# Optimization experiments

Hardware: AMD Instinct MI355X
Metric: run time of the kernel (lower is better)

The kernel has to match this reference:

```python
import jax, jax.numpy as jnp
import numpy as np

N_ATOMS, N_NBH, N_IN, N_FILTERS, N_OUT, N_GAUSS = 10000, 48, 128, 128, 128, 25
R_CUTOFF = 5.0
LOG2 = float(np.log(2.0))


def ssp(v):
    # shifted softplus, the SchNet activation
    return jax.nn.softplus(v) - LOG2


def setup_inputs() -> dict:
    key = jax.random.key(0)
    ks = jax.random.split(key, 10)
    x = jax.random.normal(ks[0], (N_ATOMS, N_IN), dtype=jnp.float32)
    dR = jax.random.uniform(ks[1], (N_ATOMS, N_NBH), dtype=jnp.float32) * 10.0  # distances in [0,10)
    dR_expanded = jax.random.normal(ks[2], (N_ATOMS, N_NBH, N_GAUSS), dtype=jnp.float32)
    pairwise_mask = jnp.ones((N_ATOMS, N_NBH), dtype=jnp.float32)
    neighbors_idx = jax.random.randint(ks[3], (N_ATOMS, N_NBH), 0, N_ATOMS, dtype=jnp.int32)
    s = 1.0 / np.sqrt(N_FILTERS)
    W1 = jax.random.normal(ks[4], (N_GAUSS, N_FILTERS), dtype=jnp.float32) * (1.0 / np.sqrt(N_GAUSS))
    b1 = jnp.zeros((N_FILTERS,), dtype=jnp.float32)
    W2 = jax.random.normal(ks[5], (N_FILTERS, N_FILTERS), dtype=jnp.float32) * s
    b2 = jnp.zeros((N_FILTERS,), dtype=jnp.float32)
    W_in2f = jax.random.normal(ks[6], (N_IN, N_FILTERS), dtype=jnp.float32) * (1.0 / np.sqrt(N_IN))
    W_f2out = jax.random.normal(ks[7], (N_FILTERS, N_OUT), dtype=jnp.float32) * s
    b_f2out = jnp.zeros((N_OUT,), dtype=jnp.float32)
    return {"x": x, "dR": dR, "dR_expanded": dR_expanded, "pairwise_mask": pairwise_mask,
            "neighbors_idx": neighbors_idx, "W1": W1, "b1": b1, "W2": W2, "b2": b2,
            "W_in2f": W_in2f, "W_f2out": W_f2out, "b_f2out": b_f2out}


def reference(x, dR, dR_expanded, pairwise_mask, neighbors_idx,
              W1, b1, W2, b2, W_in2f, W_f2out, b_f2out):
    # FilterNetwork: Dense + ssp + Dense, on Gaussian-smeared distances -> [N, K, F]
    W = jnp.einsum('nkg,gf->nkf', dR_expanded, W1) + b1
    W = jnp.einsum('nkf,fh->nkh', ssp(W), W2) + b2
    # HardCutoff: 1 where within cutoff
    C = (dR <= R_CUTOFF).astype(W.dtype)           # [N, K]
    W = W * C[..., None]
    # in2f (no bias), gather neighbor features
    y = x @ W_in2f                                  # [N, F]
    y = jnp.take(y, neighbors_idx, axis=0)          # [N, K, F] (gather == take_along_axis path)
    # filter-weighted multiply + masked sum aggregation over neighbor axis
    y = y * W
    y = jnp.sum(y * pairwise_mask[..., None], axis=1)  # [N, F]
    # f2out: Linear + shifted softplus
    return ssp(y @ W_f2out + b_f2out)               # [N, n_out]
```

## Files before the change

kernel.cpp:

```cpp
#include <hip/hip_runtime.h>
#include <hip/hip_bf16.h>


#define NA 10000
#define NK 48
#define NF 128
#define DREP 40
#define HP   136

typedef __bf16 bf16x8 __attribute__((ext_vector_type(8)));
typedef float  f32x4  __attribute__((ext_vector_type(4)));

__device__ __forceinline__ unsigned short f2bs(float x) {
    return __builtin_bit_cast(unsigned short, (__bf16)x);
}
__device__ __forceinline__ float bs2f(unsigned short u) {
    return (float)__builtin_bit_cast(__bf16, u);
}
__device__ __forceinline__ float sspf(float v) {
    return fmaxf(v, 0.0f) + __logf(1.0f + __expf(-fabsf(v))) - 0.69314718056f;
}

__global__ __launch_bounds__(256) void prep_weights(
    const float* __restrict__ W1,
    const float* __restrict__ W2,
    const float* __restrict__ Wi,
    unsigned short* __restrict__ wsb)
{
    int i = blockIdx.x * 256 + threadIdx.x;
    if (i < 4096) {
        int f = i >> 5, g = i & 31;
        wsb[i] = (g < 25) ? f2bs(W1[g * NF + f]) : (unsigned short)0;
    } else if (i < 20480) {
        int j = i - 4096; int h = j >> 7, k = j & 127;
        wsb[i] = f2bs(W2[k * NF + h]);
    } else if (i < 36864) {
        int j = i - 20480; int f = j >> 7, k = j & 127;
        wsb[i] = f2bs(Wi[k * NF + f]);
    }
}

__global__ __launch_bounds__(256) void in2f_mfma(
    const float* __restrict__ x,
    const unsigned short* __restrict__ WiT,
    unsigned short* __restrict__ yfeatb)
{
    const int tid = threadIdx.x;
    const int w = tid >> 6;
    const int lane = tid & 63;
    const int r = lane & 15;
    const int q = lane >> 4;
    const int m0 = blockIdx.x * 64 + w * 16;
    const int row = m0 + r;
    const bool rv = (row < NA);

    f32x4 acc[8];
    #pragma unroll
    for (int nt = 0; nt < 8; ++nt) { acc[nt][0]=0.f; acc[nt][1]=0.f; acc[nt][2]=0.f; acc[nt][3]=0.f; }

    #pragma unroll
    for (int ks = 0; ks < 4; ++ks) {
        bf16x8 a;
        if (rv) {
            const float4* xp = (const float4*)(x + (size_t)row * NF + ks * 32 + q * 8);
            float4 v0 = xp[0], v1 = xp[1];
            a[0]=(__bf16)v0.x; a[1]=(__bf16)v0.y; a[2]=(__bf16)v0.z; a[3]=(__bf16)v0.w;
            a[4]=(__bf16)v1.x; a[5]=(__bf16)v1.y; a[6]=(__bf16)v1.z; a[7]=(__bf16)v1.w;
        } else {
            #pragma unroll
            for (int j = 0; j < 8; ++j) a[j] = (__bf16)0.0f;
        }
        #pragma unroll
        for (int nt = 0; nt < 8; ++nt) {
            bf16x8 b = *(const bf16x8*)(WiT + (nt * 16 + r) * NF + ks * 32 + q * 8);
            acc[nt] = __builtin_amdgcn_mfma_f32_16x16x32_bf16(a, b, acc[nt], 0, 0, 0);
        }
    }
    #pragma unroll
    for (int nt = 0; nt < 8; ++nt) {
        #pragma unroll
        for (int reg = 0; reg < 4; ++reg) {
            int orow = m0 + q * 4 + reg;
            if (orow < NA)
                yfeatb[(size_t)orow * NF + nt * 16 + r] = f2bs(acc[nt][reg]);
        }
    }
}

__global__ __launch_bounds__(256) void cfconv_mfma(
    const float* __restrict__ dR,
    const float* __restrict__ dRe,
    const float* __restrict__ mask,
    const int*   __restrict__ nbr,
    const float* __restrict__ b1,
    const float* __restrict__ b2,
    const float* __restrict__ Wf2o,
    const float* __restrict__ bf2o,
    const unsigned short* __restrict__ W1T,
    const unsigned short* __restrict__ W2T,
    const unsigned short* __restrict__ yfeatb,
    float* __restrict__ out)
{
    __shared__ __align__(16) unsigned short s_dre[NK * DREP];
    __shared__ __align__(16) unsigned short s_H[NK * HP];
    __shared__ __align__(16) float s_y[NF];
    __shared__ __align__(16) float s_part[256];
    __shared__ float s_cm[NK];
    __shared__ int   s_nb[NK];

    const int tid = threadIdx.x;
    const int n = blockIdx.x;
    const int w = tid >> 6;
    const int lane = tid & 63;
    const int r = lane & 15;
    const int q = lane >> 4;
    const int nt0 = w * 2;

    {
        unsigned int* z = (unsigned int*)s_dre;
        for (int i = tid; i < NK * DREP / 2; i += 256) z[i] = 0u;
    }
    if (tid < NK) {
        float d = dR[n * NK + tid];
        float m = mask[n * NK + tid];
        s_cm[tid] = (d <= 5.0f) ? m : 0.0f;
        s_nb[tid] = nbr[n * NK + tid] * NF;
    }
    __syncthreads();
    {
        const float* dre = dRe + (size_t)n * (NK * 25);
        for (int i = tid; i < NK * 25; i += 256) {
            int k = i / 25;
            int g = i - k * 25;
            s_dre[k * DREP + g] = f2bs(dre[i]);
        }
    }
    __syncthreads();

    const float bias1a = b1[nt0 * 16 + r];
    const float bias1b = b1[nt0 * 16 + 16 + r];
    {
        bf16x8 bfr[2];
        bfr[0] = *(const bf16x8*)(W1T + ((nt0    ) * 16 + r) * 32 + q * 8);
        bfr[1] = *(const bf16x8*)(W1T + ((nt0 + 1) * 16 + r) * 32 + q * 8);
        #pragma unroll
        for (int mt = 0; mt < 3; ++mt) {
            bf16x8 a = *(const bf16x8*)(&s_dre[(mt * 16 + r) * DREP + q * 8]);
            #pragma unroll
            for (int t = 0; t < 2; ++t) {
                f32x4 zf; zf[0]=0.f; zf[1]=0.f; zf[2]=0.f; zf[3]=0.f;
                f32x4 h = __builtin_amdgcn_mfma_f32_16x16x32_bf16(a, bfr[t], zf, 0, 0, 0);
                float bia = t ? bias1b : bias1a;
                #pragma unroll
                for (int reg = 0; reg < 4; ++reg) {
                    int k = mt * 16 + q * 4 + reg;
                    int f = (nt0 + t) * 16 + r;
                    s_H[k * HP + f] = f2bs(sspf(h[reg] + bia));
                }
            }
        }
    }
    __syncthreads();

    const float bias2a = b2[nt0 * 16 + r];
    const float bias2b = b2[nt0 * 16 + 16 + r];
    f32x4 acc[3][2];
    #pragma unroll
    for (int mt = 0; mt < 3; ++mt)
        #pragma unroll
        for (int t = 0; t < 2; ++t) { acc[mt][t][0]=0.f; acc[mt][t][1]=0.f; acc[mt][t][2]=0.f; acc[mt][t][3]=0.f; }

    bf16x8 bw[2][4];
    #pragma unroll
    for (int t = 0; t < 2; ++t)
        #pragma unroll
        for (int ks = 0; ks < 4; ++ks)
            bw[t][ks] = *(const bf16x8*)(W2T + ((nt0 + t) * 16 + r) * NF + ks * 32 + q * 8);

    #pragma unroll
    for (int ks = 0; ks < 4; ++ks) {
        #pragma unroll
        for (int mt = 0; mt < 3; ++mt) {
            bf16x8 a = *(const bf16x8*)(&s_H[(mt * 16 + r) * HP + ks * 32 + q * 8]);
            #pragma unroll
            for (int t = 0; t < 2; ++t)
                acc[mt][t] = __builtin_amdgcn_mfma_f32_16x16x32_bf16(a, bw[t][ks], acc[mt][t], 0, 0, 0);
        }
    }

    float part0 = 0.f, part1 = 0.f;
    const int h0 = nt0 * 16 + r;
    #pragma unroll
    for (int mt = 0; mt < 3; ++mt) {
        #pragma unroll
        for (int reg = 0; reg < 4; ++reg) {
            int k = mt * 16 + q * 4 + reg;
            float cmk = s_cm[k];
            int base = s_nb[k];
            part0 += cmk * (acc[mt][0][reg] + bias2a) * bs2f(yfeatb[base + h0]);
            part1 += cmk * (acc[mt][1][reg] + bias2b) * bs2f(yfeatb[base + h0 + 16]);
        }
    }
    part0 += __shfl_xor(part0, 16);
    part0 += __shfl_xor(part0, 32);
    part1 += __shfl_xor(part1, 16);
    part1 += __shfl_xor(part1, 32);
    if (q == 0) {
        s_y[h0] = part0;
        s_y[h0 + 16] = part1;
    }
    __syncthreads();

    {
        int f = tid & 127;
        int half = tid >> 7;
        float o = 0.f;
        const float* wp = Wf2o + (size_t)(half * 64) * NF + f;
        const float* yp = s_y + half * 64;
        #pragma unroll 8
        for (int i = 0; i < 64; ++i)
            o = fmaf(yp[i], wp[(size_t)i * NF], o);
        s_part[tid] = o;
    }
    __syncthreads();
    if (tid < NF)
        out[(size_t)n * NF + tid] = sspf(s_part[tid] + s_part[tid + 128] + bf2o[tid]);
}

extern "C" void kernel_launch(void* const* d_in, const int* in_sizes, int n_in,
                              void* d_out, int out_size, void* d_ws, size_t ws_size,
                              hipStream_t stream)
{
    const float* x    = (const float*)d_in[0];
    const float* dR   = (const float*)d_in[1];
    const float* dRe  = (const float*)d_in[2];
    const float* mask = (const float*)d_in[3];
    const int*   nbr  = (const int*)d_in[4];
    const float* W1   = (const float*)d_in[5];
    const float* b1   = (const float*)d_in[6];
    const float* W2   = (const float*)d_in[7];
    const float* b2   = (const float*)d_in[8];
    const float* Wi2f = (const float*)d_in[9];
    const float* Wf2o = (const float*)d_in[10];
    const float* bf2o = (const float*)d_in[11];
    float* out = (float*)d_out;

    unsigned short* wsb = (unsigned short*)d_ws;
    unsigned short* W1T    = wsb;
    unsigned short* W2T    = wsb + 4096;
    unsigned short* WiT    = wsb + 20480;
    unsigned short* yfeatb = wsb + 36864;

    prep_weights<<<144, 256, 0, stream>>>(W1, W2, Wi2f, wsb);
    in2f_mfma<<<157, 256, 0, stream>>>(x, WiT, yfeatb);
    cfconv_mfma<<<NA, 256, 0, stream>>>(dR, dRe, mask, nbr, b1, b2, Wf2o, bf2o,
                                        W1T, W2T, yfeatb, out);
}
```

Baseline: 197.0 us.

## Process four atoms per cfconv block and split in2f across waves by columns

The cfconv kernel now handles four atoms per block. Weight fragments and biases are loaded into registers once per block, and the final f2out GEMV reuses each Wf2o load across four atoms. The in2f kernel is reorganized so each block covers 16 rows, with each wave computing two 16-column tiles, and the launch grows to 625 blocks. The trade-off is fewer cfconv blocks (2500), serialized per-atom phases with extra barriers inside the loop, and more shared memory per block.

Result: slower. 204.2 us (+3.6%).

```diff
diff --git a/kernel.cpp b/kernel.cpp
--- a/kernel.cpp
+++ b/kernel.cpp
@@ -5,6 +5,7 @@
 #define NA 10000
 #define NK 48
 #define NF 128
+#define AT 4
 #define DREP 40
 #define HP   136
 
@@ -50,41 +51,33 @@
     const int lane = tid & 63;
     const int r = lane & 15;
     const int q = lane >> 4;
-    const int m0 = blockIdx.x * 64 + w * 16;
-    const int row = m0 + r;
-    const bool rv = (row < NA);
-
-    f32x4 acc[8];
-    #pragma unroll
-    for (int nt = 0; nt < 8; ++nt) { acc[nt][0]=0.f; acc[nt][1]=0.f; acc[nt][2]=0.f; acc[nt][3]=0.f; }
-
+    const int nt0 = w * 2;
+    const int m0 = blockIdx.x * 16;
+
+    bf16x8 a[4];
     #pragma unroll
     for (int ks = 0; ks < 4; ++ks) {
-        bf16x8 a;
-        if (rv) {
-            const float4* xp = (const float4*)(x + (size_t)row * NF + ks * 32 + q * 8);
-            float4 v0 = xp[0], v1 = xp[1];
-            a[0]=(__bf16)v0.x; a[1]=(__bf16)v0.y; a[2]=(__bf16)v0.z; a[3]=(__bf16)v0.w;
-            a[4]=(__bf16)v1.x; a[5]=(__bf16)v1.y; a[6]=(__bf16)v1.z; a[7]=(__bf16)v1.w;
-        } else {
-            #pragma unroll
-            for (int j = 0; j < 8; ++j) a[j] = (__bf16)0.0f;
-        }
-        #pragma unroll
-        for (int nt = 0; nt < 8; ++nt) {
-            bf16x8 b = *(const bf16x8*)(WiT + (nt * 16 + r) * NF + ks * 32 + q * 8);
-            acc[nt] = __builtin_amdgcn_mfma_f32_16x16x32_bf16(a, b, acc[nt], 0, 0, 0);
-        }
-    }
-    #pragma unroll
-    for (int nt = 0; nt < 8; ++nt) {
-        #pragma unroll
-        for (int reg = 0; reg < 4; ++reg) {
-            int orow = m0 + q * 4 + reg;
-            if (orow < NA)
-                yfeatb[(size_t)orow * NF + nt * 16 + r] = f2bs(acc[nt][reg]);
-        }
-    }
+        const float4* xp = (const float4*)(x + (size_t)(m0 + r) * NF + ks * 32 + q * 8);
+        float4 v0 = xp[0], v1 = xp[1];
+        a[ks][0]=(__bf16)v0.x; a[ks][1]=(__bf16)v0.y; a[ks][2]=(__bf16)v0.z; a[ks][3]=(__bf16)v0.w;
+        a[ks][4]=(__bf16)v1.x; a[ks][5]=(__bf16)v1.y; a[ks][6]=(__bf16)v1.z; a[ks][7]=(__bf16)v1.w;
+    }
+
+    f32x4 acc[2];
+    acc[0] = (f32x4){0.f,0.f,0.f,0.f};
+    acc[1] = (f32x4){0.f,0.f,0.f,0.f};
+    #pragma unroll
+    for (int ks = 0; ks < 4; ++ks) {
+        bf16x8 b0 = *(const bf16x8*)(WiT + ((nt0    ) * 16 + r) * NF + ks * 32 + q * 8);
+        bf16x8 b1 = *(const bf16x8*)(WiT + ((nt0 + 1) * 16 + r) * NF + ks * 32 + q * 8);
+        acc[0] = __builtin_amdgcn_mfma_f32_16x16x32_bf16(a[ks], b0, acc[0], 0, 0, 0);
+        acc[1] = __builtin_amdgcn_mfma_f32_16x16x32_bf16(a[ks], b1, acc[1], 0, 0, 0);
+    }
+    #pragma unroll
+    for (int t = 0; t < 2; ++t)
+        #pragma unroll
+        for (int reg = 0; reg < 4; ++reg)
+            yfeatb[(size_t)(m0 + q * 4 + reg) * NF + (nt0 + t) * 16 + r] = f2bs(acc[t][reg]);
 }
 
 __global__ __launch_bounds__(256) void cfconv_mfma(
@@ -103,128 +96,142 @@
 {
     __shared__ __align__(16) unsigned short s_dre[NK * DREP];
     __shared__ __align__(16) unsigned short s_H[NK * HP];
-    __shared__ __align__(16) float s_y[NF];
-    __shared__ __align__(16) float s_part[256];
+    __shared__ __align__(16) float s_y4[AT][NF];
+    __shared__ __align__(16) float s_part[AT][256];
     __shared__ float s_cm[NK];
     __shared__ int   s_nb[NK];
 
     const int tid = threadIdx.x;
-    const int n = blockIdx.x;
     const int w = tid >> 6;
     const int lane = tid & 63;
     const int r = lane & 15;
     const int q = lane >> 4;
     const int nt0 = w * 2;
+    const int n0 = blockIdx.x * AT;
+
+    const float bias1a = b1[nt0 * 16 + r];
+    const float bias1b = b1[nt0 * 16 + 16 + r];
+    const float bias2a = b2[nt0 * 16 + r];
+    const float bias2b = b2[nt0 * 16 + 16 + r];
+    bf16x8 bfr0 = *(const bf16x8*)(W1T + ((nt0    ) * 16 + r) * 32 + q * 8);
+    bf16x8 bfr1 = *(const bf16x8*)(W1T + ((nt0 + 1) * 16 + r) * 32 + q * 8);
+    bf16x8 bw[2][4];
+    #pragma unroll
+    for (int t = 0; t < 2; ++t)
+        #pragma unroll
+        for (int ks = 0; ks < 4; ++ks)
+            bw[t][ks] = *(const bf16x8*)(W2T + ((nt0 + t) * 16 + r) * NF + ks * 32 + q * 8);
 
     {
         unsigned int* z = (unsigned int*)s_dre;
         for (int i = tid; i < NK * DREP / 2; i += 256) z[i] = 0u;
     }
-    if (tid < NK) {
-        float d = dR[n * NK + tid];
-        float m = mask[n * NK + tid];
-        s_cm[tid] = (d <= 5.0f) ? m : 0.0f;
-        s_nb[tid] = nbr[n * NK + tid] * NF;
-    }
     __syncthreads();
-    {
-        const float* dre = dRe + (size_t)n * (NK * 25);
-        for (int i = tid; i < NK * 25; i += 256) {
-            int k = i / 25;
-            int g = i - k * 25;
-            s_dre[k * DREP + g] = f2bs(dre[i]);
-        }
-    }
-    __syncthreads();
-
-    const float bias1a = b1[nt0 * 16 + r];
-    const float bias1b = b1[nt0 * 16 + 16 + r];
-    {
-        bf16x8 bfr[2];
-        bfr[0] = *(const bf16x8*)(W1T + ((nt0    ) * 16 + r) * 32 + q * 8);
-        bfr[1] = *(const bf16x8*)(W1T + ((nt0 + 1) * 16 + r) * 32 + q * 8);
+
+    for (int a = 0; a < AT; ++a) {
+        const int n = n0 + a;
+
+        if (tid < NK) {
+            float d = dR[n * NK + tid];
+            float m = mask[n * NK + tid];
+            s_cm[tid] = (d <= 5.0f) ? m : 0.0f;
+            s_nb[tid] = nbr[n * NK + tid] * NF;
+        }
+        {
+            const float* dre = dRe + (size_t)n * (NK * 25);
+            #pragma unroll
+            for (int i = tid; i < NK * 25; i += 256) {
+                int k = i / 25;
+                int g = i - k * 25;
+                s_dre[k * DREP + g] = f2bs(dre[i]);
+            }
+        }
+        __syncthreads();
+
         #pragma unroll
         for (int mt = 0; mt < 3; ++mt) {
-            bf16x8 a = *(const bf16x8*)(&s_dre[(mt * 16 + r) * DREP + q * 8]);
-            #pragma unroll
-            for (int t = 0; t < 2; ++t) {
-                f32x4 zf; zf[0]=0.f; zf[1]=0.f; zf[2]=0.f; zf[3]=0.f;
-                f32x4 h = __builtin_amdgcn_mfma_f32_16x16x32_bf16(a, bfr[t], zf, 0, 0, 0);
-                float bia = t ? bias1b : bias1a;
-                #pragma unroll
-                for (int reg = 0; reg < 4; ++reg) {
-                    int k = mt * 16 + q * 4 + reg;
-                    int f = (nt0 + t) * 16 + r;
-                    s_H[k * HP + f] = f2bs(sspf(h[reg] + bia));
-                }
-            }
-        }
-    }
-    __syncthreads();
-
-    const float bias2a = b2[nt0 * 16 + r];
-    const float bias2b = b2[nt0 * 16 + 16 + r];
-    f32x4 acc[3][2];
-    #pragma unroll
-    for (int mt = 0; mt < 3; ++mt)
-        #pragma unroll
-        for (int t = 0; t < 2; ++t) { acc[mt][t][0]=0.f; acc[mt][t][1]=0.f; acc[mt][t][2]=0.f; acc[mt][t][3]=0.f; }
-
-    bf16x8 bw[2][4];
-    #pragma unroll
-    for (int t = 0; t < 2; ++t)
-        #pragma unroll
-        for (int ks = 0; ks < 4; ++ks)
-            bw[t][ks] = *(const bf16x8*)(W2T + ((nt0 + t) * 16 + r) * NF + ks * 32 + q * 8);
-
-    #pragma unroll
-    for (int ks = 0; ks < 4; ++ks) {
+            bf16x8 af = *(const bf16x8*)(&s_dre[(mt * 16 + r) * DREP + q * 8]);
+            f32x4 zf = (f32x4){0.f,0.f,0.f,0.f};
+            f32x4 h0 = __builtin_amdgcn_mfma_f32_16x16x32_bf16(af, bfr0, zf, 0, 0, 0);
+            f32x4 h1 = __builtin_amdgcn_mfma_f32_16x16x32_bf16(af, bfr1, zf, 0, 0, 0);
+            #pragma unroll
+            for (int reg = 0; reg < 4; ++reg) {
+                int k = mt * 16 + q * 4 + reg;
+                s_H[k * HP + nt0 * 16 + r]      = f2bs(sspf(h0[reg] + bias1a));
+                s_H[k * HP + nt0 * 16 + 16 + r] = f2bs(sspf(h1[reg] + bias1b));
+            }
+        }
+        __syncthreads();
+
+        f32x4 acc[3][2];
         #pragma unroll
         for (int mt = 0; mt < 3; ++mt) {
-            bf16x8 a = *(const bf16x8*)(&s_H[(mt * 16 + r) * HP + ks * 32 + q * 8]);
-            #pragma unroll
-            for (int t = 0; t < 2; ++t)
-                acc[mt][t] = __builtin_amdgcn_mfma_f32_16x16x32_bf16(a, bw[t][ks], acc[mt][t], 0, 0, 0);
-        }
-    }
-
-    float part0 = 0.f, part1 = 0.f;
-    const int h0 = nt0 * 16 + r;
-    #pragma unroll
-    for (int mt = 0; mt < 3; ++mt) {
-        #pragma unroll
-        for (int reg = 0; reg < 4; ++reg) {
-            int k = mt * 16 + q * 4 + reg;
-            float cmk = s_cm[k];
-            int base = s_nb[k];
-            part0 += cmk * (acc[mt][0][reg] + bias2a) * bs2f(yfeatb[base + h0]);
-            part1 += cmk * (acc[mt][1][reg] + bias2b) * bs2f(yfeatb[base + h0 + 16]);
-        }
-    }
-    part0 += __shfl_xor(part0, 16);
-    part0 += __shfl_xor(part0, 32);
-    part1 += __shfl_xor(part1, 16);
-    part1 += __shfl_xor(part1, 32);
-    if (q == 0) {
-        s_y[h0] = part0;
-        s_y[h0 + 16] = part1;
-    }
-    __syncthreads();
+            acc[mt][0] = (f32x4){0.f,0.f,0.f,0.f};
+            acc[mt][1] = (f32x4){0.f,0.f,0.f,0.f};
+        }
+        #pragma unroll
+        for (int ks = 0; ks < 4; ++ks) {
+            #pragma unroll
+            for (int mt = 0; mt < 3; ++mt) {
+                bf16x8 af = *(const bf16x8*)(&s_H[(mt * 16 + r) * HP + ks * 32 + q * 8]);
+                acc[mt][0] = __builtin_amdgcn_mfma_f32_16x16x32_bf16(af, bw[0][ks], acc[mt][0], 0, 0, 0);
+                acc[mt][1] = __builtin_amdgcn_mfma_f32_16x16x32_bf16(af, bw[1][ks], acc[mt][1], 0, 0, 0);
+            }
+        }
+
+        float part0 = 0.f, part1 = 0.f;
+        const int h0i = nt0 * 16 + r;
+        #pragma unroll
+        for (int mt = 0; mt < 3; ++mt) {
+            #pragma unroll
+            for (int reg = 0; reg < 4; ++reg) {
+                int k = mt * 16 + q * 4 + reg;
+                float cmk = s_cm[k];
+                int base = s_nb[k];
+                part0 = fmaf(cmk * (acc[mt][0][reg] + bias2a), bs2f(yfeatb[base + h0i]), part0);
+                part1 = fmaf(cmk * (acc[mt][1][reg] + bias2b), bs2f(yfeatb[base + h0i + 16]), part1);
+            }
+        }
+        part0 += __shfl_xor(part0, 16);
+        part0 += __shfl_xor(part0, 32);
+        part1 += __shfl_xor(part1, 16);
+        part1 += __shfl_xor(part1, 32);
+        if (q == 0) {
+            s_y4[a][h0i] = part0;
+            s_y4[a][h0i + 16] = part1;
+        }
+        __syncthreads();
+    }
 
     {
         int f = tid & 127;
         int half = tid >> 7;
-        float o = 0.f;
+        float o0 = 0.f, o1 = 0.f, o2 = 0.f, o3 = 0.f;
         const float* wp = Wf2o + (size_t)(half * 64) * NF + f;
-        const float* yp = s_y + half * 64;
+        const float* y0 = &s_y4[0][half * 64];
+        const float* y1 = &s_y4[1][half * 64];
+        const float* y2 = &s_y4[2][half * 64];
+        const float* y3 = &s_y4[3][half * 64];
         #pragma unroll 8
-        for (int i = 0; i < 64; ++i)
-            o = fmaf(yp[i], wp[(size_t)i * NF], o);
-        s_part[tid] = o;
+        for (int i = 0; i < 64; ++i) {
+            float wv = wp[(size_t)i * NF];
+            o0 = fmaf(y0[i], wv, o0);
+            o1 = fmaf(y1[i], wv, o1);
+            o2 = fmaf(y2[i], wv, o2);
+            o3 = fmaf(y3[i], wv, o3);
+        }
+        s_part[0][tid] = o0;
+        s_part[1][tid] = o1;
+        s_part[2][tid] = o2;
+        s_part[3][tid] = o3;
     }
     __syncthreads();
-    if (tid < NF)
-        out[(size_t)n * NF + tid] = sspf(s_part[tid] + s_part[tid + 128] + bf2o[tid]);
+    if (tid < NF) {
+        float bo = bf2o[tid];
+        #pragma unroll
+        for (int a = 0; a < AT; ++a)
+            out[(size_t)(n0 + a) * NF + tid] = sspf(s_part[a][tid] + s_part[a][tid + 128] + bo);
+    }
 }
 
 extern "C" void kernel_launch(void* const* d_in, const int* in_sizes, int n_in,
@@ -252,7 +259,7 @@
     unsigned short* yfeatb = wsb + 36864;
 
     prep_weights<<<144, 256, 0, stream>>>(W1, W2, Wi2f, wsb);
-    in2f_mfma<<<157, 256, 0, stream>>>(x, WiT, yfeatb);
-    cfconv_mfma<<<NA, 256, 0, stream>>>(dR, dRe, mask, nbr, b1, b2, Wf2o, bf2o,
-                                        W1T, W2T, yfeatb, out);
-}
+    in2f_mfma<<<625, 256, 0, stream>>>(x, WiT, yfeatb);
+    cfconv_mfma<<<NA / AT, 256, 0, stream>>>(dR, dRe, mask, nbr, b1, b2, Wf2o, bf2o,
+                                             W1T, W2T, yfeatb, out);
+}
```
